# Kernel optimization log

Measured on AMD Instinct MI355X. Metric: run time of the kernel, lower is better.

Reference implementation:

```python
import jax, jax.numpy as jnp
import numpy as np

N_NODES = 100000

def setup_inputs() -> dict:
    key = jax.random.key(0)
    k1, k2, k3, k4, k5 = jax.random.split(key, 5)
    node_emb = jax.random.normal(k1, (100000, 128), dtype=jnp.float32)
    edge_weight = jax.random.uniform(k2, (1600000,), dtype=jnp.float32)
    src = jax.random.randint(k3, (1600000,), 0, 100000, dtype=jnp.int32)
    dst = jax.random.randint(k4, (1600000,), 0, 100000, dtype=jnp.int32)
    W = jax.random.normal(k5, (128, 128), dtype=jnp.float32) * (1.0 / np.sqrt(128))
    return {"node_emb": node_emb, "edge_weight": edge_weight, "src": src, "dst": dst, "W": W}

def reference(node_emb, edge_weight, src, dst, W):
    # u_mul_e: gather source features, scale by per-edge scalar weight
    msg = node_emb[src] * edge_weight[:, None]          # [E, d]
    # sum reduce into destination nodes (scatter-add / segment-sum)
    agg = jax.ops.segment_sum(msg, dst, num_segments=N_NODES)  # [N, d]
    # linear_out (no bias): agg @ W^T (torch Linear applies x @ W.T)
    return agg @ W.T
```

## Files before the change

kernel.cpp:

```cpp
#include <hip/hip_runtime.h>
#include <cstdint>

typedef unsigned short u16;
typedef unsigned int   u32;

#define DIM     128
#define TPITCH  136
#define BSH     9
#define BSIZE   512
#define NBK_MAX 256
#define CHUNK   8192

__device__ __forceinline__ u16 f2bf(float x) {
    u32 u = __float_as_uint(x);
    u32 r = u + 0x7FFFu + ((u >> 16) & 1u);
    return (u16)(r >> 16);
}

typedef __attribute__((ext_vector_type(8))) short bfrag;
typedef __attribute__((ext_vector_type(4))) float f32x4;

__global__ __launch_bounds__(256) void k_count_transform(
    const float* __restrict__ A, const float* __restrict__ W,
    u16* __restrict__ Tb,
    const int* __restrict__ dst, int* __restrict__ cnt,
    int n, int E, int nCntBlk, int NBK)
{
    __shared__ u16 Wb[DIM * TPITCH];

    if (blockIdx.x < nCntBlk) {
        int* hist = (int*)Wb;
        for (int i = threadIdx.x; i < NBK; i += 256) hist[i] = 0;
        __syncthreads();
        const int base = blockIdx.x * CHUNK;
        const int end  = min(base + CHUNK, E);
        for (int i = base + threadIdx.x; i < end; i += 256)
            atomicAdd(&hist[dst[i] >> BSH], 1);
        __syncthreads();
        for (int b = threadIdx.x; b < NBK; b += 256)
            cnt[b * nCntBlk + blockIdx.x] = hist[b];
        return;
    }

    {
        const int j  = threadIdx.x >> 1;
        const int k0 = (threadIdx.x & 1) << 6;
        const float* wr = W + j * DIM + k0;
        u16* wo = Wb + j * TPITCH + k0;
#pragma unroll
        for (int k = 0; k < 64; k += 4) {
            float4 v = *(const float4*)(wr + k);
            ushort4 h;
            h.x = f2bf(v.x); h.y = f2bf(v.y); h.z = f2bf(v.z); h.w = f2bf(v.w);
            *(ushort4*)(wo + k) = h;
        }
    }
    __syncthreads();

    const int wave = threadIdx.x >> 6;
    const int lane = threadIdx.x & 63;
    const int quad = lane >> 4;
    const int l16  = lane & 15;

    const int r0 = (((blockIdx.x - nCntBlk) << 2) + wave) << 4;
    if (r0 >= n) return;

    const int ar = min(r0 + l16, n - 1);
    const float* arow = A + (size_t)ar * DIM;

    f32x4 acc[8];
#pragma unroll
    for (int c = 0; c < 8; ++c) acc[c] = (f32x4)(0.f);

#pragma unroll
    for (int s = 0; s < 4; ++s) {
        const int koff = (s << 5) + (quad << 3);
        const float4 f0 = *(const float4*)(arow + koff);
        const float4 f1 = *(const float4*)(arow + koff + 4);
        bfrag a;
        a[0] = (short)f2bf(f0.x); a[1] = (short)f2bf(f0.y);
        a[2] = (short)f2bf(f0.z); a[3] = (short)f2bf(f0.w);
        a[4] = (short)f2bf(f1.x); a[5] = (short)f2bf(f1.y);
        a[6] = (short)f2bf(f1.z); a[7] = (short)f2bf(f1.w);
#pragma unroll
        for (int c = 0; c < 8; ++c) {
            const int nn = (c << 4) + l16;
            const bfrag b = *(const bfrag*)(Wb + nn * TPITCH + koff);
            acc[c] = __builtin_amdgcn_mfma_f32_16x16x32_bf16(a, b, acc[c], 0, 0, 0);
        }
    }

#pragma unroll
    for (int r = 0; r < 4; ++r) {
        const int row = r0 + (quad << 2) + r;
        if (row < n) {
            u16* orow = Tb + (size_t)row * DIM + l16;
#pragma unroll
            for (int c = 0; c < 8; ++c)
                orow[c << 4] = f2bf(acc[c][r]);
        }
    }
}

__global__ __launch_bounds__(256) void k_rowsum(
    const int* __restrict__ cnt, int* __restrict__ tot, int nCntBlk)
{
    __shared__ int red[256];
    const int t = threadIdx.x;
    const int* row = cnt + blockIdx.x * nCntBlk;
    int s = 0;
    for (int i = t; i < nCntBlk; i += 256) s += row[i];
    red[t] = s; __syncthreads();
    for (int o = 128; o; o >>= 1) {
        if (t < o) red[t] += red[t + o];
        __syncthreads();
    }
    if (t == 0) tot[blockIdx.x] = red[0];
}

__global__ __launch_bounds__(256) void k_scan_buckets(
    const int* __restrict__ tot, int* __restrict__ bucketStart, int NBK, int E)
{
    __shared__ int sc[256];
    const int t = threadIdx.x;
    const int v = (t < NBK) ? tot[t] : 0;
    sc[t] = v; __syncthreads();
    for (int d = 1; d < 256; d <<= 1) {
        int u = (t >= d) ? sc[t - d] : 0;
        __syncthreads();
        sc[t] += u;
        __syncthreads();
    }
    if (t < NBK) bucketStart[t] = sc[t] - v;
    if (t == 0) bucketStart[NBK] = E;
}

__global__ __launch_bounds__(256) void k_rowscan(
    int* __restrict__ cnt, const int* __restrict__ bucketStart, int nCntBlk)
{
    __shared__ int sc[256];
    const int t = threadIdx.x;
    int* row = cnt + blockIdx.x * nCntBlk;
    const int v = (t < nCntBlk) ? row[t] : 0;
    sc[t] = v; __syncthreads();
    for (int d = 1; d < 256; d <<= 1) {
        int u = (t >= d) ? sc[t - d] : 0;
        __syncthreads();
        sc[t] += u;
        __syncthreads();
    }
    if (t < nCntBlk) row[t] = bucketStart[blockIdx.x] + sc[t] - v;
}

__global__ __launch_bounds__(256) void k_scatter(
    const int* __restrict__ src, const int* __restrict__ dst,
    const float* __restrict__ w, const int* __restrict__ cnt,
    int2* __restrict__ es1, int E, int nCntBlk, int NBK)
{
    __shared__ int lpos[NBK_MAX];
    for (int b = threadIdx.x; b < NBK; b += 256)
        lpos[b] = cnt[b * nCntBlk + blockIdx.x];
    __syncthreads();
    const int base = blockIdx.x * CHUNK;
    const int end  = min(base + CHUNK, E);
    for (int i = base + threadIdx.x; i < end; i += 256) {
        const int d = dst[i];
        const int p = atomicAdd(&lpos[d >> BSH], 1);
        es1[p] = make_int2(src[i] | ((d & (BSIZE - 1)) << 20),
                           __float_as_int(w[i]));
    }
}

__global__ __launch_bounds__(256) void k_fine(
    const int2* __restrict__ es1, const int* __restrict__ bucketStart,
    int2* __restrict__ es2, int* __restrict__ off, int n, int NBK)
{
    __shared__ int c[BSIZE];
    __shared__ int cur[BSIZE];
    __shared__ int sums[256];

    const int b = blockIdx.x;
    const int s = bucketStart[b], e = bucketStart[b + 1];
    const int t = threadIdx.x;

    c[2 * t] = 0; c[2 * t + 1] = 0;
    __syncthreads();
    for (int i = s + t; i < e; i += 256)
        atomicAdd(&c[es1[i].x >> 20], 1);
    __syncthreads();

    const int c0 = c[2 * t], c1 = c[2 * t + 1];
    const int ts = c0 + c1;
    sums[t] = ts; __syncthreads();
    for (int d = 1; d < 256; d <<= 1) {
        int v = (t >= d) ? sums[t - d] : 0;
        __syncthreads();
        sums[t] += v;
        __syncthreads();
    }
    const int pre = sums[t] - ts;
    const int p0 = s + pre, p1 = s + pre + c0;
    cur[2 * t] = p0; cur[2 * t + 1] = p1;

    const int v0 = (b << BSH) + 2 * t, v1 = v0 + 1;
    if (v0 < n) off[v0] = p0;
    if (v1 < n) off[v1] = p1;
    if (b == NBK - 1 && t == 0) off[n] = e;
    __syncthreads();

    for (int i = s + t; i < e; i += 256) {
        const int2 ev = es1[i];
        const int p = atomicAdd(&cur[ev.x >> 20], 1);
        es2[p] = make_int2(ev.x & 0xFFFFF, ev.y);
    }
}

__global__ __launch_bounds__(256) void gnn_aggregate(
    const u16* __restrict__ Tb, const int* __restrict__ off,
    const int2* __restrict__ es, float* __restrict__ out, int n)
{
    const int v = blockIdx.x * 4 + (threadIdx.x >> 6);
    if (v >= n) return;
    const int lane = threadIdx.x & 63;
    const u32* Tw = (const u32*)Tb;

    const int b = off[v], e = off[v + 1];
    float ax = 0.f, ay = 0.f;

    int i = b;
    for (; i + 3 < e; i += 4) {
        const int2 e0 = es[i], e1 = es[i + 1], e2 = es[i + 2], e3 = es[i + 3];
        const u32 t0 = Tw[(size_t)e0.x * 64 + lane];
        const u32 t1 = Tw[(size_t)e1.x * 64 + lane];
        const u32 t2 = Tw[(size_t)e2.x * 64 + lane];
        const u32 t3 = Tw[(size_t)e3.x * 64 + lane];
        const float w0 = __int_as_float(e0.y), w1 = __int_as_float(e1.y);
        const float w2 = __int_as_float(e2.y), w3 = __int_as_float(e3.y);
        ax += w0 * __uint_as_float(t0 << 16);
        ay += w0 * __uint_as_float(t0 & 0xFFFF0000u);
        ax += w1 * __uint_as_float(t1 << 16);
        ay += w1 * __uint_as_float(t1 & 0xFFFF0000u);
        ax += w2 * __uint_as_float(t2 << 16);
        ay += w2 * __uint_as_float(t2 & 0xFFFF0000u);
        ax += w3 * __uint_as_float(t3 << 16);
        ay += w3 * __uint_as_float(t3 & 0xFFFF0000u);
    }
    for (; i < e; ++i) {
        const int2 ev = es[i];
        const u32 t = Tw[(size_t)ev.x * 64 + lane];
        const float w = __int_as_float(ev.y);
        ax += w * __uint_as_float(t << 16);
        ay += w * __uint_as_float(t & 0xFFFF0000u);
    }

    *(float2*)(out + (size_t)v * DIM + 2 * lane) = make_float2(ax, ay);
}

extern "C" void kernel_launch(void* const* d_in, const int* in_sizes, int n_in,
                              void* d_out, int out_size, void* d_ws, size_t ws_size,
                              hipStream_t stream)
{
    const float* node_emb = (const float*)d_in[0];
    const float* ew       = (const float*)d_in[1];
    const int*   src      = (const int*)d_in[2];
    const int*   dst      = (const int*)d_in[3];
    const float* W        = (const float*)d_in[4];
    float* out = (float*)d_out;

    const int n = in_sizes[0] / DIM;
    const int E = in_sizes[1];
    const int NBK = (n + BSIZE - 1) >> BSH;
    const int nCntBlk = (E + CHUNK - 1) / CHUNK;
    const int M = NBK * nCntBlk;

    char* ws = (char*)d_ws;
    size_t o = 0;
    u16* Tb = (u16*)(ws + o);  o += (((size_t)n * DIM * sizeof(u16)) + 255) & ~255ULL;
    int* cnt = (int*)(ws + o); o += (((size_t)M * sizeof(int)) + 255) & ~255ULL;
    int* tot = (int*)(ws + o); o += (((size_t)NBK * sizeof(int)) + 255) & ~255ULL;
    int* bucketStart = (int*)(ws + o); o += (((size_t)(NBK + 1) * sizeof(int)) + 255) & ~255ULL;
    int* off = (int*)(ws + o); o += (((size_t)(n + 1) * sizeof(int)) + 255) & ~255ULL;
    int2* es1 = (int2*)(ws + o); o += (((size_t)E * sizeof(int2)) + 255) & ~255ULL;
    int2* es2 = (int2*)(ws + o);

    const int ntiles = (n + 63) >> 6;

    k_count_transform<<<nCntBlk + ntiles, 256, 0, stream>>>(
        node_emb, W, Tb, dst, cnt, n, E, nCntBlk, NBK);

    k_rowsum<<<NBK, 256, 0, stream>>>(cnt, tot, nCntBlk);
    k_scan_buckets<<<1, 256, 0, stream>>>(tot, bucketStart, NBK, E);
    k_rowscan<<<NBK, 256, 0, stream>>>(cnt, bucketStart, nCntBlk);

    k_scatter<<<nCntBlk, 256, 0, stream>>>(src, dst, ew, cnt, es1, E, nCntBlk, NBK);

    k_fine<<<NBK, 256, 0, stream>>>(es1, bucketStart, es2, off, n, NBK);

    gnn_aggregate<<<(n + 3) / 4, 256, 0, stream>>>(Tb, off, es2, out, n);
}
```

Before: 267.6 us.

## Stage scatter in LDS for coalesced writes, widen fine sort, persistent aggregate

k_scatter now sorts each chunk's edges by bucket in shared memory first, then writes them to es1 in contiguous runs. This replaces scattered global writes with mostly coalesced ones. k_fine moves to 512 threads, one per destination slot, using a 512-wide scan. gnn_aggregate becomes a grid-stride kernel of 2048 blocks with an 8-way unrolled gather, two accumulator pairs to expose more loads in flight, and nontemporal output stores. The cost is large LDS use in k_scatter (about 73KB), which limits occupancy.

```diff
diff --git a/kernel.cpp b/kernel.cpp
--- a/kernel.cpp
+++ b/kernel.cpp
@@ -3,6 +3,7 @@
 
 typedef unsigned short u16;
 typedef unsigned int   u32;
+typedef unsigned char  u8;
 
 #define DIM     128
 #define TPITCH  136
@@ -19,6 +20,7 @@
 
 typedef __attribute__((ext_vector_type(8))) short bfrag;
 typedef __attribute__((ext_vector_type(4))) float f32x4;
+typedef __attribute__((ext_vector_type(2))) float f32x2;
 
 __global__ __launch_bounds__(256) void k_count_transform(
     const float* __restrict__ A, const float* __restrict__ W,
@@ -152,66 +154,103 @@
     if (t < nCntBlk) row[t] = bucketStart[blockIdx.x] + sc[t] - v;
 }
 
-__global__ __launch_bounds__(256) void k_scatter(
+__global__ __launch_bounds__(512) void k_scatter(
     const int* __restrict__ src, const int* __restrict__ dst,
     const float* __restrict__ w, const int* __restrict__ cnt,
+    const int* __restrict__ bucketStart,
     int2* __restrict__ es1, int E, int nCntBlk, int NBK)
 {
-    __shared__ int lpos[NBK_MAX];
-    for (int b = threadIdx.x; b < NBK; b += 256)
-        lpos[b] = cnt[b * nCntBlk + blockIdx.x];
-    __syncthreads();
-    const int base = blockIdx.x * CHUNK;
+    __shared__ int2 buf[CHUNK];
+    __shared__ u8   bid[CHUNK];
+    __shared__ int  gbase[NBK_MAX];
+    __shared__ int  lbase[NBK_MAX];
+    __shared__ int  lpos[NBK_MAX];
+    __shared__ int  sc[256];
+
+    const int blk  = blockIdx.x;
+    const int base = blk * CHUNK;
     const int end  = min(base + CHUNK, E);
-    for (int i = base + threadIdx.x; i < end; i += 256) {
-        const int d = dst[i];
-        const int p = atomicAdd(&lpos[d >> BSH], 1);
-        es1[p] = make_int2(src[i] | ((d & (BSIZE - 1)) << 20),
+    const int len  = end - base;
+    const int t    = threadIdx.x;
+
+    int mylen = 0;
+    if (t < NBK) {
+        const int g = cnt[t * nCntBlk + blk];
+        gbase[t] = g;
+        const int nxt = (blk + 1 < nCntBlk) ? cnt[t * nCntBlk + blk + 1]
+                                            : bucketStart[t + 1];
+        mylen = nxt - g;
+    }
+    if (t < 256) sc[t] = (t < NBK) ? mylen : 0;
+    __syncthreads();
+    for (int d = 1; d < 256; d <<= 1) {
+        int v = 0;
+        if (t < 256 && t >= d) v = sc[t - d];
+        __syncthreads();
+        if (t < 256) sc[t] += v;
+        __syncthreads();
+    }
+    if (t < NBK) {
+        const int ex = sc[t] - mylen;
+        lbase[t] = ex;
+        lpos[t]  = ex;
+    }
+    __syncthreads();
+
+    for (int i = base + t; i < end; i += 512) {
+        const int d   = dst[i];
+        const int bkt = d >> BSH;
+        const int p   = atomicAdd(&lpos[bkt], 1);
+        buf[p] = make_int2(src[i] | ((d & (BSIZE - 1)) << 20),
                            __float_as_int(w[i]));
-    }
-}
-
-__global__ __launch_bounds__(256) void k_fine(
+        bid[p] = (u8)bkt;
+    }
+    __syncthreads();
+
+    for (int i = t; i < len; i += 512) {
+        const int bkt = bid[i];
+        es1[gbase[bkt] + (i - lbase[bkt])] = buf[i];
+    }
+}
+
+__global__ __launch_bounds__(512) void k_fine(
     const int2* __restrict__ es1, const int* __restrict__ bucketStart,
     int2* __restrict__ es2, int* __restrict__ off, int n, int NBK)
 {
     __shared__ int c[BSIZE];
     __shared__ int cur[BSIZE];
-    __shared__ int sums[256];
+    __shared__ int sc[BSIZE];
 
     const int b = blockIdx.x;
     const int s = bucketStart[b], e = bucketStart[b + 1];
     const int t = threadIdx.x;
 
-    c[2 * t] = 0; c[2 * t + 1] = 0;
-    __syncthreads();
-    for (int i = s + t; i < e; i += 256)
+    c[t] = 0;
+    __syncthreads();
+    for (int i = s + t; i < e; i += 512)
         atomicAdd(&c[es1[i].x >> 20], 1);
     __syncthreads();
 
-    const int c0 = c[2 * t], c1 = c[2 * t + 1];
-    const int ts = c0 + c1;
-    sums[t] = ts; __syncthreads();
-    for (int d = 1; d < 256; d <<= 1) {
-        int v = (t >= d) ? sums[t - d] : 0;
-        __syncthreads();
-        sums[t] += v;
-        __syncthreads();
-    }
-    const int pre = sums[t] - ts;
-    const int p0 = s + pre, p1 = s + pre + c0;
-    cur[2 * t] = p0; cur[2 * t + 1] = p1;
-
-    const int v0 = (b << BSH) + 2 * t, v1 = v0 + 1;
-    if (v0 < n) off[v0] = p0;
-    if (v1 < n) off[v1] = p1;
+    const int myc = c[t];
+    sc[t] = myc; __syncthreads();
+    for (int d = 1; d < 512; d <<= 1) {
+        int v = (t >= d) ? sc[t - d] : 0;
+        __syncthreads();
+        sc[t] += v;
+        __syncthreads();
+    }
+    const int p = s + sc[t] - myc;
+    cur[t] = p;
+
+    const int v0 = (b << BSH) + t;
+    if (v0 < n) off[v0] = p;
     if (b == NBK - 1 && t == 0) off[n] = e;
     __syncthreads();
 
-    for (int i = s + t; i < e; i += 256) {
+    for (int i = s + t; i < e; i += 512) {
         const int2 ev = es1[i];
-        const int p = atomicAdd(&cur[ev.x >> 20], 1);
-        es2[p] = make_int2(ev.x & 0xFFFFF, ev.y);
+        const int pp = atomicAdd(&cur[ev.x >> 20], 1);
+        es2[pp] = make_int2(ev.x & 0xFFFFF, ev.y);
     }
 }
 
@@ -219,41 +258,81 @@
     const u16* __restrict__ Tb, const int* __restrict__ off,
     const int2* __restrict__ es, float* __restrict__ out, int n)
 {
-    const int v = blockIdx.x * 4 + (threadIdx.x >> 6);
-    if (v >= n) return;
     const int lane = threadIdx.x & 63;
-    const u32* Tw = (const u32*)Tb;
-
-    const int b = off[v], e = off[v + 1];
-    float ax = 0.f, ay = 0.f;
-
-    int i = b;
-    for (; i + 3 < e; i += 4) {
-        const int2 e0 = es[i], e1 = es[i + 1], e2 = es[i + 2], e3 = es[i + 3];
-        const u32 t0 = Tw[(size_t)e0.x * 64 + lane];
-        const u32 t1 = Tw[(size_t)e1.x * 64 + lane];
-        const u32 t2 = Tw[(size_t)e2.x * 64 + lane];
-        const u32 t3 = Tw[(size_t)e3.x * 64 + lane];
-        const float w0 = __int_as_float(e0.y), w1 = __int_as_float(e1.y);
-        const float w2 = __int_as_float(e2.y), w3 = __int_as_float(e3.y);
-        ax += w0 * __uint_as_float(t0 << 16);
-        ay += w0 * __uint_as_float(t0 & 0xFFFF0000u);
-        ax += w1 * __uint_as_float(t1 << 16);
-        ay += w1 * __uint_as_float(t1 & 0xFFFF0000u);
-        ax += w2 * __uint_as_float(t2 << 16);
-        ay += w2 * __uint_as_float(t2 & 0xFFFF0000u);
-        ax += w3 * __uint_as_float(t3 << 16);
-        ay += w3 * __uint_as_float(t3 & 0xFFFF0000u);
-    }
-    for (; i < e; ++i) {
-        const int2 ev = es[i];
-        const u32 t = Tw[(size_t)ev.x * 64 + lane];
-        const float w = __int_as_float(ev.y);
-        ax += w * __uint_as_float(t << 16);
-        ay += w * __uint_as_float(t & 0xFFFF0000u);
-    }
-
-    *(float2*)(out + (size_t)v * DIM + 2 * lane) = make_float2(ax, ay);
+    const int wv   = threadIdx.x >> 6;
+    const u32* Tw  = (const u32*)Tb;
+    const int ngrp = (n + 3) >> 2;
+
+    for (int g = blockIdx.x; g < ngrp; g += gridDim.x) {
+        const int v = (g << 2) + wv;
+        if (v >= n) continue;
+
+        const int b = off[v], e = off[v + 1];
+        float ax0 = 0.f, ay0 = 0.f, ax1 = 0.f, ay1 = 0.f;
+
+        int i = b;
+        for (; i + 7 < e; i += 8) {
+            const int2 e0 = es[i],     e1 = es[i + 1], e2 = es[i + 2], e3 = es[i + 3];
+            const int2 e4 = es[i + 4], e5 = es[i + 5], e6 = es[i + 6], e7 = es[i + 7];
+            const u32 t0 = Tw[(size_t)e0.x * 64 + lane];
+            const u32 t1 = Tw[(size_t)e1.x * 64 + lane];
+            const u32 t2 = Tw[(size_t)e2.x * 64 + lane];
+            const u32 t3 = Tw[(size_t)e3.x * 64 + lane];
+            const u32 t4 = Tw[(size_t)e4.x * 64 + lane];
+            const u32 t5 = Tw[(size_t)e5.x * 64 + lane];
+            const u32 t6 = Tw[(size_t)e6.x * 64 + lane];
+            const u32 t7 = Tw[(size_t)e7.x * 64 + lane];
+            const float w0 = __int_as_float(e0.y), w1 = __int_as_float(e1.y);
+            const float w2 = __int_as_float(e2.y), w3 = __int_as_float(e3.y);
+            const float w4 = __int_as_float(e4.y), w5 = __int_as_float(e5.y);
+            const float w6 = __int_as_float(e6.y), w7 = __int_as_float(e7.y);
+            ax0 += w0 * __uint_as_float(t0 << 16);
+            ay0 += w0 * __uint_as_float(t0 & 0xFFFF0000u);
+            ax1 += w1 * __uint_as_float(t1 << 16);
+            ay1 += w1 * __uint_as_float(t1 & 0xFFFF0000u);
+            ax0 += w2 * __uint_as_float(t2 << 16);
+            ay0 += w2 * __uint_as_float(t2 & 0xFFFF0000u);
+            ax1 += w3 * __uint_as_float(t3 << 16);
+            ay1 += w3 * __uint_as_float(t3 & 0xFFFF0000u);
+            ax0 += w4 * __uint_as_float(t4 << 16);
+            ay0 += w4 * __uint_as_float(t4 & 0xFFFF0000u);
+            ax1 += w5 * __uint_as_float(t5 << 16);
+            ay1 += w5 * __uint_as_float(t5 & 0xFFFF0000u);
+            ax0 += w6 * __uint_as_float(t6 << 16);
+            ay0 += w6 * __uint_as_float(t6 & 0xFFFF0000u);
+            ax1 += w7 * __uint_as_float(t7 << 16);
+            ay1 += w7 * __uint_as_float(t7 & 0xFFFF0000u);
+        }
+        for (; i + 3 < e; i += 4) {
+            const int2 e0 = es[i], e1 = es[i + 1], e2 = es[i + 2], e3 = es[i + 3];
+            const u32 t0 = Tw[(size_t)e0.x * 64 + lane];
+            const u32 t1 = Tw[(size_t)e1.x * 64 + lane];
+            const u32 t2 = Tw[(size_t)e2.x * 64 + lane];
+            const u32 t3 = Tw[(size_t)e3.x * 64 + lane];
+            const float w0 = __int_as_float(e0.y), w1 = __int_as_float(e1.y);
+            const float w2 = __int_as_float(e2.y), w3 = __int_as_float(e3.y);
+            ax0 += w0 * __uint_as_float(t0 << 16);
+            ay0 += w0 * __uint_as_float(t0 & 0xFFFF0000u);
+            ax1 += w1 * __uint_as_float(t1 << 16);
+            ay1 += w1 * __uint_as_float(t1 & 0xFFFF0000u);
+            ax0 += w2 * __uint_as_float(t2 << 16);
+            ay0 += w2 * __uint_as_float(t2 & 0xFFFF0000u);
+            ax1 += w3 * __uint_as_float(t3 << 16);
+            ay1 += w3 * __uint_as_float(t3 & 0xFFFF0000u);
+        }
+        for (; i < e; ++i) {
+            const int2 ev = es[i];
+            const u32 t = Tw[(size_t)ev.x * 64 + lane];
+            const float w0 = __int_as_float(ev.y);
+            ax0 += w0 * __uint_as_float(t << 16);
+            ay0 += w0 * __uint_as_float(t & 0xFFFF0000u);
+        }
+
+        f32x2 r;
+        r[0] = ax0 + ax1;
+        r[1] = ay0 + ay1;
+        __builtin_nontemporal_store(r, (f32x2*)(out + (size_t)v * DIM + 2 * lane));
+    }
 }
 
 extern "C" void kernel_launch(void* const* d_in, const int* in_sizes, int n_in,
@@ -292,9 +371,10 @@
     k_scan_buckets<<<1, 256, 0, stream>>>(tot, bucketStart, NBK, E);
     k_rowscan<<<NBK, 256, 0, stream>>>(cnt, bucketStart, nCntBlk);
 
-    k_scatter<<<nCntBlk, 256, 0, stream>>>(src, dst, ew, cnt, es1, E, nCntBlk, NBK);
-
-    k_fine<<<NBK, 256, 0, stream>>>(es1, bucketStart, es2, off, n, NBK);
-
-    gnn_aggregate<<<(n + 3) / 4, 256, 0, stream>>>(Tb, off, es2, out, n);
-}
+    k_scatter<<<nCntBlk, 512, 0, stream>>>(src, dst, ew, cnt, bucketStart,
+                                           es1, E, nCntBlk, NBK);
+
+    k_fine<<<NBK, 512, 0, stream>>>(es1, bucketStart, es2, off, n, NBK);
+
+    gnn_aggregate<<<2048, 256, 0, stream>>>(Tb, off, es2, out, n);
+}
```

New measurement: 243.4 us. -9.0%, faster.
